# Performance work log

Measured on AMD Instinct MI355X. Metric: run time of the kernel, lower is better.

The kernel has to match this reference:

```python
import jax, jax.numpy as jnp
import numpy as np

MAX_LEN = 8192  # static bound on per-row nonzeros (jit-friendly stand-in for data-dependent max_len)
B, D, E = 256, 65536, 128
DENSITY = 0.08  # expected nnz/row ~5243 << MAX_LEN


def setup_inputs() -> dict:
    key = jax.random.key(0)
    k1, k2, k3 = jax.random.split(key, 3)
    mask = jax.random.uniform(k1, (B, D)) < DENSITY
    x = jnp.where(mask, jax.random.normal(k2, (B, D), dtype=jnp.float32), 0.0)
    embed_table = jax.random.normal(k3, (D + 1, E), dtype=jnp.float32) * 0.02
    t = jnp.zeros((1,), dtype=jnp.float32)
    return {"t": t, "x": x, "embed_table": embed_table}


def reference(t, x, embed_table):
    # --- condense: per-row stream compaction of nonzero entries ---
    d = x.shape[1]
    mask = x != 0
    idx = jnp.arange(d)
    # push positions of zero entries to the end, keep nonzero positions sorted ascending
    keys = jnp.where(mask, idx, d)              # (B, D)
    order = jnp.sort(keys, axis=1)[:, :MAX_LEN]  # (B, MAX_LEN) compacted nonzero positions (pad = d)
    valid = order < d
    p = jnp.where(valid, order + 1, 0)           # 1-based positions, 0 = pad (matches torch code)
    v = jnp.where(valid, jnp.take_along_axis(x, jnp.minimum(order, d - 1), axis=1), 0.0)
    # --- embedding lookup on condensed positions (computed as in original; unused by output) ---
    id_embed = embed_table[p]                    # (B, MAX_LEN, E)
    # --- decondense: scatter values back to dense layout ---
    rows = jnp.arange(x.shape[0])[:, None]
    tgt = jnp.where(p > 0, p - 1, 0)
    y = jnp.zeros_like(x).at[rows, tgt].add(jnp.where(p > 0, v, 0.0))
    return y
```

## Files before the change

kernel.cpp:

```cpp
#include <hip/hip_runtime.h>

#define NROWS   256
#define DCOLS   65536
#define MAXLEN  8192
#define TPB     1024
#define V4PT    16
#define NWAVE   (TPB / 64)

__global__ __launch_bounds__(TPB) void condense_roundtrip_kernel(
        const float* __restrict__ x, float* __restrict__ y) {
    const int row  = blockIdx.x;
    const int t    = threadIdx.x;
    const int lane = t & 63;
    const int wave = t >> 6;

    const float4* __restrict__ x4 =
        reinterpret_cast<const float4*>(x + (size_t)row * DCOLS);
    float4* __restrict__ y4 =
        reinterpret_cast<float4*>(y + (size_t)row * DCOLS);

    float4 v[V4PT];
    int cnt = 0;
#pragma unroll
    for (int i = 0; i < V4PT; ++i) {
        v[i] = x4[i * TPB + t];
        cnt += (v[i].x != 0.0f) + (v[i].y != 0.0f) +
               (v[i].z != 0.0f) + (v[i].w != 0.0f);
    }

    int s = cnt;
#pragma unroll
    for (int off = 32; off; off >>= 1) s += __shfl_xor(s, off, 64);

    __shared__ int wsum[NWAVE];
    __shared__ int wbase[NWAVE];
    __shared__ int nnz_sh;
    if (lane == 0) wsum[wave] = s;
    __syncthreads();
    if (t == 0) {
        int acc = 0;
#pragma unroll
        for (int w = 0; w < NWAVE; ++w) acc += wsum[w];
        nnz_sh = acc;
    }
    __syncthreads();
    const int nnz = nnz_sh;

    if (nnz <= MAXLEN) {
#pragma unroll
        for (int i = 0; i < V4PT; ++i) y4[i * TPB + t] = v[i];
        return;
    }

    const float4* __restrict__ xc = x4 + t * V4PT;
    float4* __restrict__ yc = y4 + t * V4PT;

    int ccnt = 0;
#pragma unroll
    for (int i = 0; i < V4PT; ++i) {
        float4 w = xc[i];
        ccnt += (w.x != 0.0f) + (w.y != 0.0f) + (w.z != 0.0f) + (w.w != 0.0f);
    }
    int incl = ccnt;
#pragma unroll
    for (int off = 1; off < 64; off <<= 1) {
        int n = __shfl_up(incl, off, 64);
        if (lane >= off) incl += n;
    }
    if (lane == 63) wsum[wave] = incl;
    __syncthreads();
    if (t == 0) {
        int acc = 0;
#pragma unroll
        for (int w = 0; w < NWAVE; ++w) { wbase[w] = acc; acc += wsum[w]; }
    }
    __syncthreads();
    int rank = wbase[wave] + (incl - ccnt);

#pragma unroll
    for (int i = 0; i < V4PT; ++i) {
        float4 w = xc[i];
        float4 o;
        bool nx = (w.x != 0.0f); o.x = (nx && rank < MAXLEN) ? w.x : 0.0f; rank += nx;
        bool ny = (w.y != 0.0f); o.y = (ny && rank < MAXLEN) ? w.y : 0.0f; rank += ny;
        bool nz = (w.z != 0.0f); o.z = (nz && rank < MAXLEN) ? w.z : 0.0f; rank += nz;
        bool nw = (w.w != 0.0f); o.w = (nw && rank < MAXLEN) ? w.w : 0.0f; rank += nw;
        yc[i] = o;
    }
}

extern "C" void kernel_launch(void* const* d_in, const int* in_sizes, int n_in,
                              void* d_out, int out_size, void* d_ws, size_t ws_size,
                              hipStream_t stream) {
    const float* x = (const float*)d_in[1];
    float* y = (float*)d_out;
    condense_roundtrip_kernel<<<NROWS, TPB, 0, stream>>>(x, y);
}
```

Measured before the change: 137.4 us.

## Split row roundtrip into fine-grained copy/count kernel plus overflow fixup kernel

Replaces the one-block-per-row kernel with two launches. The first spreads each row over 8 blocks of 256 threads, streaming x to y while counting nonzeros per block into workspace. The second reads the per-row counts and only redoes the truncating compaction for rows exceeding MAXLEN. This aims to fix low occupancy from 256 large blocks on a many-CU GPU, at the cost of an extra launch and a workspace round trip.

```diff
diff --git a/kernel.cpp b/kernel.cpp
--- a/kernel.cpp
+++ b/kernel.cpp
@@ -1,63 +1,74 @@
 #include <hip/hip_runtime.h>
 
-#define NROWS   256
-#define DCOLS   65536
-#define MAXLEN  8192
-#define TPB     1024
-#define V4PT    16
-#define NWAVE   (TPB / 64)
+#define NROWS    256
+#define DCOLS    65536
+#define MAXLEN   8192
+#define BLKROW   8
+#define K1TPB    256
+#define K1V4     8
+#define K2TPB    1024
+#define K2V4     16
+#define NWAVE2   (K2TPB / 64)
 
-__global__ __launch_bounds__(TPB) void condense_roundtrip_kernel(
-        const float* __restrict__ x, float* __restrict__ y) {
+
+__global__ __launch_bounds__(K1TPB) void copy_count_kernel(
+        const float* __restrict__ x, float* __restrict__ y,
+        int* __restrict__ blk_cnt) {
+    const int t    = threadIdx.x;
+    const int lane = t & 63;
+    const int wave = t >> 6;
+    const size_t base4 = (size_t)blockIdx.x * (K1TPB * K1V4);
+
+    const float4* __restrict__ x4 = reinterpret_cast<const float4*>(x) + base4;
+    float4* __restrict__ y4       = reinterpret_cast<float4*>(y) + base4;
+
+    int cnt = 0;
+#pragma unroll
+    for (int i = 0; i < K1V4; ++i) {
+        float4 v = x4[i * K1TPB + t];
+        cnt += (v.x != 0.0f) + (v.y != 0.0f) + (v.z != 0.0f) + (v.w != 0.0f);
+        y4[i * K1TPB + t] = v;
+    }
+
+#pragma unroll
+    for (int off = 32; off; off >>= 1) cnt += __shfl_xor(cnt, off, 64);
+
+    __shared__ int wsum[K1TPB / 64];
+    if (lane == 0) wsum[wave] = cnt;
+    __syncthreads();
+    if (t == 0) {
+        int acc = 0;
+#pragma unroll
+        for (int w = 0; w < K1TPB / 64; ++w) acc += wsum[w];
+        blk_cnt[blockIdx.x] = acc;
+    }
+}
+
+__global__ __launch_bounds__(K2TPB) void fixup_kernel(
+        const float* __restrict__ x, float* __restrict__ y,
+        const int* __restrict__ blk_cnt) {
     const int row  = blockIdx.x;
     const int t    = threadIdx.x;
     const int lane = t & 63;
     const int wave = t >> 6;
 
-    const float4* __restrict__ x4 =
-        reinterpret_cast<const float4*>(x + (size_t)row * DCOLS);
-    float4* __restrict__ y4 =
-        reinterpret_cast<float4*>(y + (size_t)row * DCOLS);
+    __shared__ int csh[BLKROW];
+    if (t < BLKROW) csh[t] = blk_cnt[row * BLKROW + t];
+    __syncthreads();
+    int nnz = 0;
+#pragma unroll
+    for (int b = 0; b < BLKROW; ++b) nnz += csh[b];
 
-    float4 v[V4PT];
-    int cnt = 0;
-#pragma unroll
-    for (int i = 0; i < V4PT; ++i) {
-        v[i] = x4[i * TPB + t];
-        cnt += (v[i].x != 0.0f) + (v[i].y != 0.0f) +
-               (v[i].z != 0.0f) + (v[i].w != 0.0f);
-    }
+    if (nnz <= MAXLEN) return;
 
-    int s = cnt;
-#pragma unroll
-    for (int off = 32; off; off >>= 1) s += __shfl_xor(s, off, 64);
-
-    __shared__ int wsum[NWAVE];
-    __shared__ int wbase[NWAVE];
-    __shared__ int nnz_sh;
-    if (lane == 0) wsum[wave] = s;
-    __syncthreads();
-    if (t == 0) {
-        int acc = 0;
-#pragma unroll
-        for (int w = 0; w < NWAVE; ++w) acc += wsum[w];
-        nnz_sh = acc;
-    }
-    __syncthreads();
-    const int nnz = nnz_sh;
-
-    if (nnz <= MAXLEN) {
-#pragma unroll
-        for (int i = 0; i < V4PT; ++i) y4[i * TPB + t] = v[i];
-        return;
-    }
-
-    const float4* __restrict__ xc = x4 + t * V4PT;
-    float4* __restrict__ yc = y4 + t * V4PT;
+    const float4* __restrict__ xc =
+        reinterpret_cast<const float4*>(x + (size_t)row * DCOLS) + t * K2V4;
+    float4* __restrict__ yc =
+        reinterpret_cast<float4*>(y + (size_t)row * DCOLS) + t * K2V4;
 
     int ccnt = 0;
 #pragma unroll
-    for (int i = 0; i < V4PT; ++i) {
+    for (int i = 0; i < K2V4; ++i) {
         float4 w = xc[i];
         ccnt += (w.x != 0.0f) + (w.y != 0.0f) + (w.z != 0.0f) + (w.w != 0.0f);
     }
@@ -67,18 +78,20 @@
         int n = __shfl_up(incl, off, 64);
         if (lane >= off) incl += n;
     }
+    __shared__ int wsum[NWAVE2];
+    __shared__ int wbase[NWAVE2];
     if (lane == 63) wsum[wave] = incl;
     __syncthreads();
     if (t == 0) {
         int acc = 0;
 #pragma unroll
-        for (int w = 0; w < NWAVE; ++w) { wbase[w] = acc; acc += wsum[w]; }
+        for (int w = 0; w < NWAVE2; ++w) { wbase[w] = acc; acc += wsum[w]; }
     }
     __syncthreads();
     int rank = wbase[wave] + (incl - ccnt);
 
 #pragma unroll
-    for (int i = 0; i < V4PT; ++i) {
+    for (int i = 0; i < K2V4; ++i) {
         float4 w = xc[i];
         float4 o;
         bool nx = (w.x != 0.0f); o.x = (nx && rank < MAXLEN) ? w.x : 0.0f; rank += nx;
@@ -94,5 +107,8 @@
                               hipStream_t stream) {
     const float* x = (const float*)d_in[1];
     float* y = (float*)d_out;
-    condense_roundtrip_kernel<<<NROWS, TPB, 0, stream>>>(x, y);
+    int* blk_cnt = (int*)d_ws;
+
+    copy_count_kernel<<<NROWS * BLKROW, K1TPB, 0, stream>>>(x, y, blk_cnt);
+    fixup_kernel<<<NROWS, K2TPB, 0, stream>>>(x, y, blk_cnt);
 }
```

Result: no change. 138.1 us (+0.5%).
